# Kernel tuning notes

Hardware: AMD Instinct MI355X
Metric: run time of the kernel (lower is better)

Reference implementation:

```python
import jax, jax.numpy as jnp
import numpy as np

POS_MARGIN = 0.9   # sample_method on
NEG_MARGIN = 0.1
EPOCH_NUM = 300
BASE = 0.5


def setup_inputs() -> dict:
    key = jax.random.key(0)
    k1, k2 = jax.random.split(key)
    n, d = 8192, 128
    x = jax.random.normal(k1, (n, d), dtype=jnp.float32)
    x = x / jnp.linalg.norm(x, axis=1, keepdims=True)  # L2-normalized embeddings
    targets = jax.random.randint(k2, (n,), 0, 100, dtype=jnp.int64 if jax.config.jax_enable_x64 else jnp.int32)
    return {"inputs": x, "targets": targets, "nonorm": 0}


def reference(inputs, targets, nonorm):
    n = inputs.shape[0]
    ep = EPOCH_NUM / 300.0  # dynamic-margin coefficient
    sim = inputs @ inputs.T  # [n, n]
    eq = targets[:, None] == targets[None, :]

    # positive pairs: same label and sim < pos_margin
    pos_mask = eq & (sim < POS_MARGIN)
    pos_min = jnp.min(jnp.where(pos_mask, sim, jnp.inf), axis=1)  # min(pos_pair_) per row

    # negative pairs: diff label, sim + 0.5 > min(pos), sim > neg_margin
    neg_mask = (~eq) & (sim + BASE > pos_min[:, None]) & (sim > NEG_MARGIN)

    pos_term = jnp.where(pos_mask, jnp.exp(-2.0 * (sim - BASE) + ep * (sim - POS_MARGIN) ** 2), 0.0)
    pos_loss = 0.5 * jnp.log1p(pos_term.sum(axis=1))
    neg_term = jnp.where(neg_mask, jnp.exp(50.0 * (sim - BASE) + ep * (NEG_MARGIN - sim) ** 2), 0.0)
    neg_loss = (1.0 / 50.0) * jnp.log1p(neg_term.sum(axis=1))

    has_neg = neg_mask.any(axis=1)  # rows with empty neg set are skipped
    loss = jnp.where(has_neg, pos_loss + neg_loss, 0.0).sum() / n
    prec = jnp.mean((~has_neg).astype(jnp.float32))

    # mean_pos_sim / mean_neg_sim come from the LAST row's filtered pairs
    last_pos = pos_mask[n - 1]
    last_neg = neg_mask[n - 1]
    mean_pos_sim = jnp.sum(jnp.where(last_pos, sim[n - 1], 0.0)) / jnp.maximum(last_pos.sum(), 1)
    mean_neg_sim = jnp.sum(jnp.where(last_neg, sim[n - 1], 0.0)) / jnp.maximum(last_neg.sum(), 1)
    return (loss, prec, mean_pos_sim, mean_neg_sim)
```

## Files before the change

### kernel.cpp

```cpp
#include <hip/hip_runtime.h>
#include <hip/hip_bf16.h>
#include <math.h>


#define D 128
#define NL 128
#define POSB NL

typedef __attribute__((ext_vector_type(8))) short short8;
typedef __attribute__((ext_vector_type(4))) float float4v;

__device__ inline float waveSum(float v) {
    #pragma unroll
    for (int o = 32; o > 0; o >>= 1) v += __shfl_down(v, o, 64);
    return v;
}

__device__ inline void load_lds16(const void* g, void* l) {
    __builtin_amdgcn_global_load_lds(
        (const __attribute__((address_space(1))) unsigned int*)g,
        (__attribute__((address_space(3))) unsigned int*)l, 16, 0, 0);
}

__global__ __launch_bounds__(512) void prep_kernel(
    const float* __restrict__ x, ushort* __restrict__ xb, int total8,
    const int* __restrict__ t, int* __restrict__ offs, int* __restrict__ list,
    float* __restrict__ part, float* __restrict__ last4,
    float* __restrict__ out, int n, int nconv)
{
    const int tid = threadIdx.x;
    const int bx = blockIdx.x;
    if (bx < nconv) {
        const int g = bx * 512 + tid;
        if (g >= total8) return;
        const float4* src = (const float4*)(x) + g * 2;
        float4 a = src[0], b = src[1];
        float f[8] = {a.x, a.y, a.z, a.w, b.x, b.y, b.z, b.w};
        ushort r[8];
        #pragma unroll
        for (int i = 0; i < 8; ++i) {
            unsigned u = __float_as_uint(f[i]);
            r[i] = (ushort)((u + 0x7FFFu + ((u >> 16) & 1u)) >> 16);
        }
        uint4 packed;
        packed.x = (unsigned)r[0] | ((unsigned)r[1] << 16);
        packed.y = (unsigned)r[2] | ((unsigned)r[3] << 16);
        packed.z = (unsigned)r[4] | ((unsigned)r[5] << 16);
        packed.w = (unsigned)r[6] | ((unsigned)r[7] << 16);
        ((uint4*)xb)[g] = packed;
        return;
    }
    if (bx > nconv) {
        const int zb = bx - nconv - 1;
        const int g4 = zb * 2048 + tid * 4;
        if (g4 < 8 * n)
            *(float4*)(part + g4) = (float4){0.f, 0.f, 0.f, 0.f};
        return;
    }
    __shared__ int cnt[NL], cur[NL];
    if (tid < 4) { last4[tid] = 0.f; out[tid] = 0.f; }
    if (tid < NL) cnt[tid] = 0;
    __syncthreads();
    for (int j = tid; j < n; j += 512) atomicAdd(&cnt[t[j]], 1);
    __syncthreads();
    if (tid == 0) {
        int acc = 0;
        for (int g = 0; g < NL; ++g) { cur[g] = acc; offs[g] = acc; acc += cnt[g]; }
        offs[NL] = acc;
    }
    __syncthreads();
    for (int j = tid; j < n; j += 512) {
        int p = atomicAdd(&cur[t[j]], 1);
        list[p] = j;
    }
}

__global__ __launch_bounds__(256, 4) void fused_kernel(
    const ushort* __restrict__ xb,
    const int* __restrict__ t,
    const int* __restrict__ offs, const int* __restrict__ list,
    float* __restrict__ pos_min, float* __restrict__ pos_sum,
    float* __restrict__ part, float* __restrict__ last4, int n)
{
    __shared__ __align__(16) unsigned char smem[32768];
    const int tid = threadIdx.x;
    const int bx = blockIdx.x;

    const int w = tid >> 6, lane = tid & 63;
    const int wy = w >> 1, wx = w & 1;
    const int quad = lane >> 4, lq = lane & 15;

    uint4* Au = (uint4*)smem;
    uint4* Bu = Au + 128 * 8;
    const uint4* xbv = (const uint4*)xb;
    const short8* As = (const short8*)Au;
    const short8* Bs = (const short8*)Bu;

    if (bx >= POSB) {
        int b = bx - POSB;
        int r = (int)((sqrtf(8.0f * (float)b + 1.0f) - 1.0f) * 0.5f);
        while ((r + 1) * (r + 2) / 2 <= b) ++r;
        while (r * (r + 1) / 2 > b) --r;
        const int c = b - r * (r + 1) / 2;
        const bool offdiag = (r != c);

        const int i0 = r * 128, j0 = c * 128;
        const bool has_last = (i0 == n - 128);

        float4v acc[4][4];
        #pragma unroll
        for (int a = 0; a < 4; ++a)
            #pragma unroll
            for (int d2 = 0; d2 < 4; ++d2) acc[a][d2] = (float4v){0.f, 0.f, 0.f, 0.f};

        #pragma unroll
        for (int h = 0; h < 2; ++h) {
            if (h) __syncthreads();
            #pragma unroll
            for (int it = 0; it < 4; ++it) {
                const int d = tid + it * 256;
                const int row = d >> 3;
                const int q = (d & 7) ^ (row & 7);
                const int ub = (d & ~63) * 16;
                load_lds16(xbv + (size_t)(i0 + row) * 16 + h * 8 + q,
                           (char*)Au + ub);
                load_lds16(xbv + (size_t)(j0 + row) * 16 + h * 8 + q,
                           (char*)Bu + ub);
            }
            __syncthreads();
            #pragma unroll
            for (int s = 0; s < 2; ++s) {
                short8 af[4], bf[4];
                #pragma unroll
                for (int tt = 0; tt < 4; ++tt) {
                    const int ra = wy * 64 + tt * 16 + lq;
                    const int rb2 = wx * 64 + tt * 16 + lq;
                    af[tt] = As[ra * 8 + ((s * 4 + quad) ^ (lq & 7))];
                    bf[tt] = Bs[rb2 * 8 + ((s * 4 + quad) ^ (lq & 7))];
                }
                #pragma unroll
                for (int tr = 0; tr < 4; ++tr)
                    #pragma unroll
                    for (int tc = 0; tc < 4; ++tc)
                        acc[tr][tc] = __builtin_amdgcn_mfma_f32_16x16x32_bf16(
                            af[tr], bf[tc], acc[tr][tc], 0, 0, 0);
            }
        }

        int lcv[4];
        #pragma unroll
        for (int tc = 0; tc < 4; ++tc) lcv[tc] = t[j0 + wx * 64 + tc * 16 + lq];
        float colp[4] = {0.f, 0.f, 0.f, 0.f};

        #pragma unroll
        for (int tr = 0; tr < 4; ++tr) {
            const int4 lr4 = *(const int4*)&t[i0 + wy * 64 + tr * 16 + quad * 4];
            float ns[4];
            #pragma unroll
            for (int reg = 0; reg < 4; ++reg) {
                const int lr = (reg == 0) ? lr4.x : (reg == 1) ? lr4.y
                             : (reg == 2) ? lr4.z : lr4.w;
                float v = 0.f;
                #pragma unroll
                for (int tc = 0; tc < 4; ++tc) {
                    const float s = acc[tr][tc][reg];
                    const bool sel = (lr != lcv[tc]) & (s > 0.1f);
                    const float e = sel
                        ? __expf(fmaf(s, s, fmaf(49.8f, s, -24.99f))) : 0.f;
                    v += e; colp[tc] += e;
                }
                ns[reg] = v;

                if (has_last && wy == 1 && tr == 3 && quad == 3 && reg == 3) {
                    float ssim = 0.f, ncf = 0.f;
                    #pragma unroll
                    for (int tc = 0; tc < 4; ++tc) {
                        const float s = acc[tr][tc][reg];
                        if ((lr != lcv[tc]) & (s > 0.1f)) { ssim += s; ncf += 1.f; }
                    }
                    #pragma unroll
                    for (int o = 1; o < 16; o <<= 1) {
                        ssim += __shfl_xor(ssim, o, 64);
                        ncf  += __shfl_xor(ncf, o, 64);
                    }
                    if (lq == 0 && ncf > 0.f) {
                        atomicAdd(&last4[2], ssim);
                        atomicAdd(&last4[3], ncf);
                    }
                }
            }
            const bool b4 = (lq & 4) != 0, b8 = (lq & 8) != 0;
            float s0 = b4 ? ns[0] : ns[2];
            float s1 = b4 ? ns[1] : ns[3];
            float r0 = (b4 ? ns[2] : ns[0]) + __shfl_xor(s0, 4, 64);
            float r1 = (b4 ? ns[3] : ns[1]) + __shfl_xor(s1, 4, 64);
            float s2 = b8 ? r0 : r1;
            float tot = (b8 ? r1 : r0) + __shfl_xor(s2, 8, 64);
            tot += __shfl_xor(tot, 1, 64);
            tot += __shfl_xor(tot, 2, 64);
            if ((lq & 3) == 0) {
                const int rr = quad * 4 + (b4 ? 2 : 0) + (b8 ? 1 : 0);
                atomicAdd(&part[(size_t)(c & 7) * n + i0 + wy * 64 + tr * 16 + rr], tot);
            }
        }
        if (offdiag) {
            #pragma unroll
            for (int tc = 0; tc < 4; ++tc) {
                float v = colp[tc];
                v += __shfl_xor(v, 16, 64);
                v += __shfl_xor(v, 32, 64);
                if (lane < 16)
                    atomicAdd(&part[(size_t)(r & 7) * n + j0 + wx * 64 + tc * 16 + lane], v);
            }
        }
        return;
    }

    const int g = bx;
    const int s0 = offs[g], m = offs[g + 1] - s0;
    if (m <= 0) return;

    const bool glast = (g == t[n - 1]);
    const int nrt = (m + 127) >> 7;

    float* posS = (float*)smem;
    float* posM = posS + 256;

    for (int rt = 0; rt < nrt; ++rt) {
        const int rbase = rt << 7;
        const int rleft = min(128, m - rbase);
        for (int ct = 0; ct < nrt; ++ct) {
            const int cbase = ct << 7;
            if (rt + ct) __syncthreads();

            float4v acc[4][4];
            #pragma unroll
            for (int a = 0; a < 4; ++a)
                #pragma unroll
                for (int d2 = 0; d2 < 4; ++d2) acc[a][d2] = (float4v){0.f, 0.f, 0.f, 0.f};

            #pragma unroll
            for (int h = 0; h < 2; ++h) {
                if (h) __syncthreads();
                #pragma unroll
                for (int it = 0; it < 4; ++it) {
                    const int d = tid + it * 256;
                    const int row = d >> 3;
                    const int q = (d & 7) ^ (row & 7);
                    const int ub = (d & ~63) * 16;
                    const int ia = list[s0 + min(rbase + row, m - 1)];
                    const int ib = list[s0 + min(cbase + row, m - 1)];
                    load_lds16(xbv + (size_t)ia * 16 + h * 8 + q,
                               (char*)Au + ub);
                    load_lds16(xbv + (size_t)ib * 16 + h * 8 + q,
                               (char*)Bu + ub);
                }
                __syncthreads();
                #pragma unroll
                for (int ks = 0; ks < 2; ++ks) {
                    short8 af[4], bf[4];
                    #pragma unroll
                    for (int tt = 0; tt < 4; ++tt) {
                        const int ra = wy * 64 + tt * 16 + lq;
                        const int rb2 = wx * 64 + tt * 16 + lq;
                        af[tt] = As[ra * 8 + ((ks * 4 + quad) ^ (lq & 7))];
                        bf[tt] = Bs[rb2 * 8 + ((ks * 4 + quad) ^ (lq & 7))];
                    }
                    #pragma unroll
                    for (int tr = 0; tr < 4; ++tr)
                        #pragma unroll
                        for (int tc = 0; tc < 4; ++tc)
                            acc[tr][tc] = __builtin_amdgcn_mfma_f32_16x16x32_bf16(
                                af[tr], bf[tc], acc[tr][tc], 0, 0, 0);
                }
            }
            __syncthreads();

            float ssl = 0.f, scl = 0.f;
            #pragma unroll
            for (int tr = 0; tr < 4; ++tr) {
                float ps[4], mnv[4];
                #pragma unroll
                for (int reg = 0; reg < 4; ++reg) {
                    const int row_loc = wy * 64 + tr * 16 + quad * 4 + reg;
                    float pv = 0.f, mn = INFINITY;
                    #pragma unroll
                    for (int tc = 0; tc < 4; ++tc) {
                        const int col = cbase + wx * 64 + tc * 16 + lq;
                        const float sv = acc[tr][tc][reg];
                        const bool val = (col < m) & (sv < 0.9f);
                        mn = fminf(mn, val ? sv : INFINITY);
                        pv += val ? __expf(fmaf(sv, sv, fmaf(-3.8f, sv, 1.81f))) : 0.f;
                    }
                    ps[reg] = pv; mnv[reg] = mn;

                    if (glast && row_loc < rleft &&
                        list[s0 + rbase + row_loc] == n - 1) {
                        #pragma unroll
                        for (int tc = 0; tc < 4; ++tc) {
                            const int col = cbase + wx * 64 + tc * 16 + lq;
                            const float sv = acc[tr][tc][reg];
                            if ((col < m) & (sv < 0.9f)) { ssl += sv; scl += 1.f; }
                        }
                    }
                }
                const bool b4 = (lq & 4) != 0, b8 = (lq & 8) != 0;
                float a0 = b4 ? ps[0] : ps[2];
                float a1 = b4 ? ps[1] : ps[3];
                float r0 = (b4 ? ps[2] : ps[0]) + __shfl_xor(a0, 4, 64);
                float r1 = (b4 ? ps[3] : ps[1]) + __shfl_xor(a1, 4, 64);
                float a2 = b8 ? r0 : r1;
                float stot = (b8 ? r1 : r0) + __shfl_xor(a2, 8, 64);
                stot += __shfl_xor(stot, 1, 64);
                stot += __shfl_xor(stot, 2, 64);

                float m0 = b4 ? mnv[0] : mnv[2];
                float m1 = b4 ? mnv[1] : mnv[3];
                float q0 = fminf(b4 ? mnv[2] : mnv[0], __shfl_xor(m0, 4, 64));
                float q1 = fminf(b4 ? mnv[3] : mnv[1], __shfl_xor(m1, 4, 64));
                float m2 = b8 ? q0 : q1;
                float mtot = fminf(b8 ? q1 : q0, __shfl_xor(m2, 8, 64));
                mtot = fminf(mtot, __shfl_xor(mtot, 1, 64));
                mtot = fminf(mtot, __shfl_xor(mtot, 2, 64));

                if ((lq & 3) == 0) {
                    const int rr = quad * 4 + (b4 ? 2 : 0) + (b8 ? 1 : 0);
                    const int row_loc = wy * 64 + tr * 16 + rr;
                    posS[wx * 128 + row_loc] = stot;
                    posM[wx * 128 + row_loc] = mtot;
                }
            }
            if (glast) {
                #pragma unroll
                for (int o = 1; o < 16; o <<= 1) {
                    ssl += __shfl_xor(ssl, o, 64);
                    scl += __shfl_xor(scl, o, 64);
                }
                if (lq == 0 && scl > 0.f) {
                    atomicAdd(&last4[0], ssl);
                    atomicAdd(&last4[1], scl);
                }
            }
            __syncthreads();

            if (tid < rleft) {
                const float stot = posS[tid] + posS[128 + tid];
                const float mtot = fminf(posM[tid], posM[128 + tid]);
                const int i = list[s0 + rbase + tid];
                if (ct == 0) { pos_sum[i] = stot; pos_min[i] = mtot; }
                else {
                    pos_sum[i] += stot;
                    pos_min[i] = fminf(pos_min[i], mtot);
                }
            }
        }
    }
}

__global__ __launch_bounds__(256) void finalize_kernel(
    const ushort* __restrict__ xb, const int* __restrict__ t,
    const float* __restrict__ pos_min, const float* __restrict__ pos_sum,
    const float* __restrict__ part, const float* __restrict__ last4,
    float* __restrict__ out, int n)
{
    const int tid = threadIdx.x;
    const int base = blockIdx.x * 256;
    const int i = base + tid;
    const float pm = pos_min[i];
    const bool flag = (pm > 0.6f);

    __shared__ int fl[256];
    __shared__ int nfl, lastflag;
    __shared__ float corr[256];
    __shared__ float xi2[D];
    __shared__ float red[3][4];
    __shared__ float lastst[2];
    if (tid == 0) { nfl = 0; lastflag = 0; }
    __syncthreads();
    if (flag) { int q = atomicAdd(&nfl, 1); fl[q] = tid; }
    __syncthreads();
    const int m = nfl;

    for (int e = 0; e < m; ++e) {
        const int lr_ = fl[e];
        const int ri = base + lr_;
        if (tid < D)
            xi2[tid] = __uint_as_float(((unsigned)xb[(size_t)ri * D + tid]) << 16);
        __syncthreads();
        const float pth = fmaxf(0.1f, pos_min[ri] - 0.5f);
        const int lab = t[ri];
        float S = 0.f, ss = 0.f, cnt = 0.f;
        for (int j = tid; j < n; j += 256) {
            if (t[j] == lab) continue;
            float d = 0.f;
            const ushort* xr = xb + (size_t)j * D;
            for (int q = 0; q < D; ++q)
                d += __uint_as_float(((unsigned)xr[q]) << 16) * xi2[q];
            if (d > pth) {
                S += __expf(fmaf(d, d, fmaf(49.8f, d, -24.99f)));
                ss += d; cnt += 1.f;
            }
        }
        const int lane = tid & 63, wv = tid >> 6;
        S = waveSum(S); ss = waveSum(ss); cnt = waveSum(cnt);
        if (lane == 0) { red[0][wv] = S; red[1][wv] = ss; red[2][wv] = cnt; }
        __syncthreads();
        if (tid == 0) {
            corr[lr_] = red[0][0] + red[0][1] + red[0][2] + red[0][3];
            if (ri == n - 1) {
                lastst[0] = red[1][0] + red[1][1] + red[1][2] + red[1][3];
                lastst[1] = red[2][0] + red[2][1] + red[2][2] + red[2][3];
                lastflag = 1;
            }
        }
        __syncthreads();
    }

    float s;
    if (flag) {
        s = corr[tid];
    } else {
        s = 0.f;
        #pragma unroll
        for (int sl = 0; sl < 8; ++sl) s += part[(size_t)sl * n + i];
    }
    float l = 0.f, nno = 0.f;
    if (s > 0.f)
        l = 0.5f * log1pf(pos_sum[i]) + 0.02f * log1pf(s);
    else
        nno = 1.f;
    const int lane = tid & 63, wv = tid >> 6;
    l = waveSum(l); nno = waveSum(nno);
    __syncthreads();
    if (lane == 0) { red[0][wv] = l; red[1][wv] = nno; }
    __syncthreads();
    if (tid == 0) {
        float L = red[0][0] + red[0][1] + red[0][2] + red[0][3];
        float P = red[1][0] + red[1][1] + red[1][2] + red[1][3];
        atomicAdd(&out[0], L / (float)n);
        atomicAdd(&out[1], P / (float)n);
    }
    if (i == n - 1) {
        out[2] = last4[0] / fmaxf(last4[1], 1.f);
        float a = lastflag ? lastst[0] : last4[2];
        float b2 = lastflag ? lastst[1] : last4[3];
        out[3] = a / fmaxf(b2, 1.f);
    }
}

extern "C" void kernel_launch(void* const* d_in, const int* in_sizes, int n_in,
                              void* d_out, int out_size, void* d_ws, size_t ws_size,
                              hipStream_t stream) {
    const float* x = (const float*)d_in[0];
    const int*   t = (const int*)d_in[1];
    const int n = in_sizes[1];

    float* ws      = (float*)d_ws;
    float* pos_min = ws;
    float* pos_sum = ws + n;
    float* last4   = ws + 2 * n;
    float* part    = ws + 2 * n + 4;
    int*   offs    = (int*)(ws + 10 * n + 4);
    int*   list    = (int*)(ws + 10 * n + 4 + NL + 1);
    size_t xb_off  = ((size_t)(11 * n + 4 + NL + 1) + 3) & ~(size_t)3;
    ushort* xb     = (ushort*)(ws + xb_off);

    const int total8 = n * D / 8;
    const int nconv = (total8 + 511) / 512;
    const int nzero = (8 * n + 2047) / 2048;
    prep_kernel<<<nconv + 1 + nzero, 512, 0, stream>>>(
        x, xb, total8, t, offs, list, part, last4, (float*)d_out, n, nconv);

    const int nb = n / 128;
    const int ntri = nb * (nb + 1) / 2;
    fused_kernel<<<POSB + ntri, 256, 0, stream>>>(
        xb, t, offs, list, pos_min, pos_sum, part, last4, n);

    finalize_kernel<<<n / 256, 256, 0, stream>>>(xb, t, pos_min, pos_sum,
                                                 part, last4, (float*)d_out, n);
}
```

Before: 101.3 us.

## Make negative-tile blocks persistent with double-buffered LDS prefetch of next tile

Turns the one-tile-per-block launch for the triangular negative-pair GEMM into 512 persistent blocks that stride over the tiles. LDS is doubled to 64KB so the next tile's first K-half loads asynchronously while the current tile's second half computes, hiding global-to-LDS latency. This halves launch-bound occupancy (4 to 2 blocks) and raises LDS per block. Positive-pair blocks share the kernel and now also get the larger LDS allocation. That may reduce residency and cause tail imbalance over roughly 2080 tiles.

```diff
diff --git a/kernel.cpp b/kernel.cpp
--- a/kernel.cpp
+++ b/kernel.cpp
@@ -6,6 +6,7 @@
 #define D 128
 #define NL 128
 #define POSB NL
+#define NEGBLKS 512
 
 typedef __attribute__((ext_vector_type(8))) short short8;
 typedef __attribute__((ext_vector_type(4))) float float4v;
@@ -20,6 +21,48 @@
     __builtin_amdgcn_global_load_lds(
         (const __attribute__((address_space(1))) unsigned int*)g,
         (__attribute__((address_space(3))) unsigned int*)l, 16, 0, 0);
+}
+
+__device__ inline void decode_tri(int b, int& r, int& c) {
+    int rr = (int)((sqrtf(8.0f * (float)b + 1.0f) - 1.0f) * 0.5f);
+    while ((rr + 1) * (rr + 2) / 2 <= b) ++rr;
+    while (rr * (rr + 1) / 2 > b) --rr;
+    r = rr; c = b - rr * (rr + 1) / 2;
+}
+
+__device__ inline void stage_half(const uint4* xbv, int i0, int j0, int h,
+                                  char* bufA, char* bufB, int tid) {
+    #pragma unroll
+    for (int it = 0; it < 4; ++it) {
+        const int d = tid + it * 256;
+        const int row = d >> 3;
+        const int q = (d & 7) ^ (row & 7);
+        const int ub = (d & ~63) * 16;
+        load_lds16(xbv + (size_t)(i0 + row) * 16 + h * 8 + q, bufA + ub);
+        load_lds16(xbv + (size_t)(j0 + row) * 16 + h * 8 + q, bufB + ub);
+    }
+}
+
+__device__ inline void compute_half(const short8* As, const short8* Bs,
+                                    int wy, int wx, int quad, int lq,
+                                    float4v acc[4][4]) {
+    #pragma unroll
+    for (int s = 0; s < 2; ++s) {
+        short8 af[4], bf[4];
+        #pragma unroll
+        for (int tt = 0; tt < 4; ++tt) {
+            const int ra = wy * 64 + tt * 16 + lq;
+            const int rb2 = wx * 64 + tt * 16 + lq;
+            af[tt] = As[ra * 8 + ((s * 4 + quad) ^ (lq & 7))];
+            bf[tt] = Bs[rb2 * 8 + ((s * 4 + quad) ^ (lq & 7))];
+        }
+        #pragma unroll
+        for (int tr = 0; tr < 4; ++tr)
+            #pragma unroll
+            for (int tc = 0; tc < 4; ++tc)
+                acc[tr][tc] = __builtin_amdgcn_mfma_f32_16x16x32_bf16(
+                    af[tr], bf[tc], acc[tr][tc], 0, 0, 0);
+    }
 }
 
 __global__ __launch_bounds__(512) void prep_kernel(
@@ -75,14 +118,14 @@
     }
 }
 
-__global__ __launch_bounds__(256, 4) void fused_kernel(
+__global__ __launch_bounds__(256, 2) void fused_kernel(
     const ushort* __restrict__ xb,
     const int* __restrict__ t,
     const int* __restrict__ offs, const int* __restrict__ list,
     float* __restrict__ pos_min, float* __restrict__ pos_sum,
-    float* __restrict__ part, float* __restrict__ last4, int n)
+    float* __restrict__ part, float* __restrict__ last4, int n, int ntri)
 {
-    __shared__ __align__(16) unsigned char smem[32768];
+    __shared__ __align__(16) unsigned char smem[65536];
     const int tid = threadIdx.x;
     const int bx = blockIdx.x;
 
@@ -90,131 +133,122 @@
     const int wy = w >> 1, wx = w & 1;
     const int quad = lane >> 4, lq = lane & 15;
 
-    uint4* Au = (uint4*)smem;
-    uint4* Bu = Au + 128 * 8;
     const uint4* xbv = (const uint4*)xb;
-    const short8* As = (const short8*)Au;
-    const short8* Bs = (const short8*)Bu;
 
     if (bx >= POSB) {
+        char* A0 = (char*)smem;
+        char* B0 = (char*)smem + 16384;
+        char* A1 = (char*)smem + 32768;
+        char* B1 = (char*)smem + 49152;
+
         int b = bx - POSB;
-        int r = (int)((sqrtf(8.0f * (float)b + 1.0f) - 1.0f) * 0.5f);
-        while ((r + 1) * (r + 2) / 2 <= b) ++r;
-        while (r * (r + 1) / 2 > b) --r;
-        const int c = b - r * (r + 1) / 2;
-        const bool offdiag = (r != c);
-
-        const int i0 = r * 128, j0 = c * 128;
-        const bool has_last = (i0 == n - 128);
-
-        float4v acc[4][4];
-        #pragma unroll
-        for (int a = 0; a < 4; ++a)
-            #pragma unroll
-            for (int d2 = 0; d2 < 4; ++d2) acc[a][d2] = (float4v){0.f, 0.f, 0.f, 0.f};
-
-        #pragma unroll
-        for (int h = 0; h < 2; ++h) {
-            if (h) __syncthreads();
-            #pragma unroll
-            for (int it = 0; it < 4; ++it) {
-                const int d = tid + it * 256;
-                const int row = d >> 3;
-                const int q = (d & 7) ^ (row & 7);
-                const int ub = (d & ~63) * 16;
-                load_lds16(xbv + (size_t)(i0 + row) * 16 + h * 8 + q,
-                           (char*)Au + ub);
-                load_lds16(xbv + (size_t)(j0 + row) * 16 + h * 8 + q,
-                           (char*)Bu + ub);
-            }
+        if (b >= ntri) return;
+        int rc, cc; decode_tri(b, rc, cc);
+        stage_half(xbv, rc * 128, cc * 128, 0, A0, B0, tid);
+
+        while (true) {
+            const int i0 = rc * 128, j0 = cc * 128;
+            const bool has_last = (i0 == n - 128);
+            const bool offdiag = (rc != cc);
+            const int bn = b + NEGBLKS;
+            const bool hasn = (bn < ntri);
+
             __syncthreads();
-            #pragma unroll
-            for (int s = 0; s < 2; ++s) {
-                short8 af[4], bf[4];
-                #pragma unroll
-                for (int tt = 0; tt < 4; ++tt) {
-                    const int ra = wy * 64 + tt * 16 + lq;
-                    const int rb2 = wx * 64 + tt * 16 + lq;
-                    af[tt] = As[ra * 8 + ((s * 4 + quad) ^ (lq & 7))];
-                    bf[tt] = Bs[rb2 * 8 + ((s * 4 + quad) ^ (lq & 7))];
-                }
-                #pragma unroll
-                for (int tr = 0; tr < 4; ++tr)
-                    #pragma unroll
-                    for (int tc = 0; tc < 4; ++tc)
-                        acc[tr][tc] = __builtin_amdgcn_mfma_f32_16x16x32_bf16(
-                            af[tr], bf[tc], acc[tr][tc], 0, 0, 0);
-            }
-        }
-
-        int lcv[4];
-        #pragma unroll
-        for (int tc = 0; tc < 4; ++tc) lcv[tc] = t[j0 + wx * 64 + tc * 16 + lq];
-        float colp[4] = {0.f, 0.f, 0.f, 0.f};
-
-        #pragma unroll
-        for (int tr = 0; tr < 4; ++tr) {
-            const int4 lr4 = *(const int4*)&t[i0 + wy * 64 + tr * 16 + quad * 4];
-            float ns[4];
-            #pragma unroll
-            for (int reg = 0; reg < 4; ++reg) {
-                const int lr = (reg == 0) ? lr4.x : (reg == 1) ? lr4.y
-                             : (reg == 2) ? lr4.z : lr4.w;
-                float v = 0.f;
-                #pragma unroll
-                for (int tc = 0; tc < 4; ++tc) {
-                    const float s = acc[tr][tc][reg];
-                    const bool sel = (lr != lcv[tc]) & (s > 0.1f);
-                    const float e = sel
-                        ? __expf(fmaf(s, s, fmaf(49.8f, s, -24.99f))) : 0.f;
-                    v += e; colp[tc] += e;
-                }
-                ns[reg] = v;
-
-                if (has_last && wy == 1 && tr == 3 && quad == 3 && reg == 3) {
-                    float ssim = 0.f, ncf = 0.f;
+            stage_half(xbv, i0, j0, 1, A1, B1, tid);
+
+            float4v acc[4][4];
+            #pragma unroll
+            for (int a = 0; a < 4; ++a)
+                #pragma unroll
+                for (int d2 = 0; d2 < 4; ++d2) acc[a][d2] = (float4v){0.f, 0.f, 0.f, 0.f};
+
+            compute_half((const short8*)A0, (const short8*)B0, wy, wx, quad, lq, acc);
+
+            __syncthreads();
+            int rn = 0, cn = 0;
+            if (hasn) {
+                decode_tri(bn, rn, cn);
+                stage_half(xbv, rn * 128, cn * 128, 0, A0, B0, tid);
+            }
+            compute_half((const short8*)A1, (const short8*)B1, wy, wx, quad, lq, acc);
+
+            int lcv[4];
+            #pragma unroll
+            for (int tc = 0; tc < 4; ++tc) lcv[tc] = t[j0 + wx * 64 + tc * 16 + lq];
+            float colp[4] = {0.f, 0.f, 0.f, 0.f};
+
+            #pragma unroll
+            for (int tr = 0; tr < 4; ++tr) {
+                const int4 lr4 = *(const int4*)&t[i0 + wy * 64 + tr * 16 + quad * 4];
+                float ns[4];
+                #pragma unroll
+                for (int reg = 0; reg < 4; ++reg) {
+                    const int lr = (reg == 0) ? lr4.x : (reg == 1) ? lr4.y
+                                 : (reg == 2) ? lr4.z : lr4.w;
+                    float v = 0.f;
                     #pragma unroll
                     for (int tc = 0; tc < 4; ++tc) {
                         const float s = acc[tr][tc][reg];
-                        if ((lr != lcv[tc]) & (s > 0.1f)) { ssim += s; ncf += 1.f; }
+                        const bool sel = (lr != lcv[tc]) & (s > 0.1f);
+                        const float e = sel
+                            ? __expf(fmaf(s, s, fmaf(49.8f, s, -24.99f))) : 0.f;
+                        v += e; colp[tc] += e;
                     }
-                    #pragma unroll
-                    for (int o = 1; o < 16; o <<= 1) {
-                        ssim += __shfl_xor(ssim, o, 64);
-                        ncf  += __shfl_xor(ncf, o, 64);
+                    ns[reg] = v;
+
+                    if (has_last && wy == 1 && tr == 3 && quad == 3 && reg == 3) {
+                        float ssim = 0.f, ncf = 0.f;
+                        #pragma unroll
+                        for (int tc = 0; tc < 4; ++tc) {
+                            const float s = acc[tr][tc][reg];
+                            if ((lr != lcv[tc]) & (s > 0.1f)) { ssim += s; ncf += 1.f; }
+                        }
+                        #pragma unroll
+                        for (int o = 1; o < 16; o <<= 1) {
+                            ssim += __shfl_xor(ssim, o, 64);
+                            ncf  += __shfl_xor(ncf, o, 64);
+                        }
+                        if (lq == 0 && ncf > 0.f) {
+                            atomicAdd(&last4[2], ssim);
+                            atomicAdd(&last4[3], ncf);
+                        }
                     }
-                    if (lq == 0 && ncf > 0.f) {
-                        atomicAdd(&last4[2], ssim);
-                        atomicAdd(&last4[3], ncf);
-                    }
-                }
-            }
-            const bool b4 = (lq & 4) != 0, b8 = (lq & 8) != 0;
-            float s0 = b4 ? ns[0] : ns[2];
-            float s1 = b4 ? ns[1] : ns[3];
-            float r0 = (b4 ? ns[2] : ns[0]) + __shfl_xor(s0, 4, 64);
-            float r1 = (b4 ? ns[3] : ns[1]) + __shfl_xor(s1, 4, 64);
-            float s2 = b8 ? r0 : r1;
-            float tot = (b8 ? r1 : r0) + __shfl_xor(s2, 8, 64);
-            tot += __shfl_xor(tot, 1, 64);
-            tot += __shfl_xor(tot, 2, 64);
-            if ((lq & 3) == 0) {
-                const int rr = quad * 4 + (b4 ? 2 : 0) + (b8 ? 1 : 0);
-                atomicAdd(&part[(size_t)(c & 7) * n + i0 + wy * 64 + tr * 16 + rr], tot);
-            }
-        }
-        if (offdiag) {
-            #pragma unroll
-            for (int tc = 0; tc < 4; ++tc) {
-                float v = colp[tc];
-                v += __shfl_xor(v, 16, 64);
-                v += __shfl_xor(v, 32, 64);
-                if (lane < 16)
-                    atomicAdd(&part[(size_t)(r & 7) * n + j0 + wx * 64 + tc * 16 + lane], v);
-            }
+                }
+                const bool b4 = (lq & 4) != 0, b8 = (lq & 8) != 0;
+                float s0 = b4 ? ns[0] : ns[2];
+                float s1 = b4 ? ns[1] : ns[3];
+                float r0 = (b4 ? ns[2] : ns[0]) + __shfl_xor(s0, 4, 64);
+                float r1 = (b4 ? ns[3] : ns[1]) + __shfl_xor(s1, 4, 64);
+                float s2 = b8 ? r0 : r1;
+                float tot = (b8 ? r1 : r0) + __shfl_xor(s2, 8, 64);
+                tot += __shfl_xor(tot, 1, 64);
+                tot += __shfl_xor(tot, 2, 64);
+                if ((lq & 3) == 0) {
+                    const int rr = quad * 4 + (b4 ? 2 : 0) + (b8 ? 1 : 0);
+                    atomicAdd(&part[(size_t)(cc & 7) * n + i0 + wy * 64 + tr * 16 + rr], tot);
+                }
+            }
+            if (offdiag) {
+                #pragma unroll
+                for (int tc = 0; tc < 4; ++tc) {
+                    float v = colp[tc];
+                    v += __shfl_xor(v, 16, 64);
+                    v += __shfl_xor(v, 32, 64);
+                    if (lane < 16)
+                        atomicAdd(&part[(size_t)(rc & 7) * n + j0 + wx * 64 + tc * 16 + lane], v);
+                }
+            }
+
+            if (!hasn) break;
+            b = bn; rc = rn; cc = cn;
         }
         return;
     }
+
+    uint4* Au = (uint4*)smem;
+    uint4* Bu = Au + 128 * 8;
+    const short8* As = (const short8*)Au;
+    const short8* Bs = (const short8*)Bu;
 
     const int g = bx;
     const int s0 = offs[g], m = offs[g + 1] - s0;
@@ -256,23 +290,7 @@
                                (char*)Bu + ub);
                 }
                 __syncthreads();
-                #pragma unroll
-                for (int ks = 0; ks < 2; ++ks) {
-                    short8 af[4], bf[4];
-                    #pragma unroll
-                    for (int tt = 0; tt < 4; ++tt) {
-                        const int ra = wy * 64 + tt * 16 + lq;
-                        const int rb2 = wx * 64 + tt * 16 + lq;
-                        af[tt] = As[ra * 8 + ((ks * 4 + quad) ^ (lq & 7))];
-                        bf[tt] = Bs[rb2 * 8 + ((ks * 4 + quad) ^ (lq & 7))];
-                    }
-                    #pragma unroll
-                    for (int tr = 0; tr < 4; ++tr)
-                        #pragma unroll
-                        for (int tc = 0; tc < 4; ++tc)
-                            acc[tr][tc] = __builtin_amdgcn_mfma_f32_16x16x32_bf16(
-                                af[tr], bf[tc], acc[tr][tc], 0, 0, 0);
-                }
+                compute_half(As, Bs, wy, wx, quad, lq, acc);
             }
             __syncthreads();
 
@@ -473,8 +491,8 @@
 
     const int nb = n / 128;
     const int ntri = nb * (nb + 1) / 2;
-    fused_kernel<<<POSB + ntri, 256, 0, stream>>>(
-        xb, t, offs, list, pos_min, pos_sum, part, last4, n);
+    fused_kernel<<<POSB + NEGBLKS, 256, 0, stream>>>(
+        xb, t, offs, list, pos_min, pos_sum, part, last4, n, ntri);
 
     finalize_kernel<<<n / 256, 256, 0, stream>>>(xb, t, pos_min, pos_sum,
                                                  part, last4, (float*)d_out, n);
```

Result: slower. 106.3 us (+5.0%).
